# Optimization experiments

Measured on AMD Instinct MI355X. Metric: run time of the kernel, lower is better.

## Reference

```python
import jax, jax.numpy as jnp
import numpy as np

B, T = 256, 64
EMBED, GRU, HID = 1024, 1024, 1024
SD, SC = 32, 32
ADIM = 6
UNIMIX = 0.01
SFLAT = SD * SC


def setup_inputs() -> dict:
    key = jax.random.key(0)
    ks = jax.random.split(key, 16)
    rn = lambda k, s: jax.random.normal(k, s, jnp.float32) * 0.02
    return {
        "embeds": jax.random.normal(ks[0], (B, T, EMBED), jnp.float32),
        "actions": jax.random.uniform(ks[1], (B, T, ADIM), jnp.float32),
        "h_init": jnp.zeros((B, GRU), jnp.float32),
        "z_init": jnp.zeros((B, SD, SC), jnp.float32),
        "W_pre": rn(ks[2], (HID, SFLAT + ADIM)), "b_pre": jnp.zeros((HID,)),
        "g_pre": jnp.ones((HID,)), "be_pre": jnp.zeros((HID,)),
        "W_ih": rn(ks[3], (3 * GRU, HID)), "W_hh": rn(ks[4], (3 * GRU, GRU)),
        "b_ih": jnp.zeros((3 * GRU,)), "b_hh": jnp.zeros((3 * GRU,)),
        "g_gn": jnp.ones((GRU,)), "b_gn": jnp.zeros((GRU,)),
        "Wp1": rn(ks[5], (HID, GRU)), "bp1": jnp.zeros((HID,)),
        "gp": jnp.ones((HID,)), "bpn": jnp.zeros((HID,)),
        "Wp2": rn(ks[6], (SFLAT, HID)), "bp2": jnp.zeros((SFLAT,)),
        "Wq1": rn(ks[7], (HID, GRU + EMBED)), "bq1": jnp.zeros((HID,)),
        "gq": jnp.ones((HID,)), "bqn": jnp.zeros((HID,)),
        "Wq2": rn(ks[8], (SFLAT, HID)), "bq2": jnp.zeros((SFLAT,)),
        # pre-drawn uniform noise -> gumbel, for categorical sampling per step
        "u_prior": jax.random.uniform(ks[9], (T, B, SD, SC), jnp.float32, 1e-6, 1.0 - 1e-6),
        "u_post": jax.random.uniform(ks[10], (T, B, SD, SC), jnp.float32, 1e-6, 1.0 - 1e-6),
    }


def _ln(x, g, b, eps=1e-5):
    m = jnp.mean(x, -1, keepdims=True)
    v = jnp.var(x, -1, keepdims=True)
    return (x - m) * jax.lax.rsqrt(v + eps) * g + b


def _mlp(x, W1, b1, g, bn, W2, b2):
    h = jax.nn.silu(_ln(x @ W1.T + b1, g, bn))
    return h @ W2.T + b2


def _sample(logits, u):
    # logits: (B, SD*SC), u: (B, SD, SC) uniform noise
    lg = logits.reshape(logits.shape[0], SD, SC)
    probs = jax.nn.softmax(lg, axis=-1)
    probs = (1.0 - UNIMIX) * probs + UNIMIX / SC
    gumbel = -jnp.log(-jnp.log(u))
    idx = jnp.argmax(jnp.log(probs) + gumbel, axis=-1)  # multinomial sample
    oh = jax.nn.one_hot(idx, SC, dtype=probs.dtype)
    z = oh + probs - jax.lax.stop_gradient(probs)  # straight-through
    return z, probs


def reference(embeds, actions, h_init, z_init,
              W_pre, b_pre, g_pre, be_pre,
              W_ih, W_hh, b_ih, b_hh, g_gn, b_gn,
              Wp1, bp1, gp, bpn, Wp2, bp2,
              Wq1, bq1, gq, bqn, Wq2, bq2,
              u_prior, u_post):
    def step(carry, xs):
        h, z = carry
        a, e, up, uq = xs
        x = jnp.concatenate([z.reshape(z.shape[0], -1), a], axis=-1)
        x = jax.nn.silu(_ln(x @ W_pre.T + b_pre, g_pre, be_pre))
        # GRUCell
        gx = x @ W_ih.T + b_ih
        gh = h @ W_hh.T + b_hh
        xr, xu, xn = jnp.split(gx, 3, axis=-1)
        hr, hu, hn = jnp.split(gh, 3, axis=-1)
        r = jax.nn.sigmoid(xr + hr)
        u_gate = jax.nn.sigmoid(xu + hu)
        n = jnp.tanh(xn + r * hn)
        h = (1.0 - u_gate) * n + u_gate * h
        h = _ln(h, g_gn, b_gn)
        prior_logits = _mlp(h, Wp1, bp1, gp, bpn, Wp2, bp2)
        _, prior_p = _sample(prior_logits, up)
        post_logits = _mlp(jnp.concatenate([h, e], axis=-1), Wq1, bq1, gq, bqn, Wq2, bq2)
        post_z, post_p = _sample(post_logits, uq)
        return (h, post_z), (h, post_z, prior_p, post_p)

    xs = (jnp.swapaxes(actions, 0, 1), jnp.swapaxes(embeds, 0, 1), u_prior, u_post)
    _, (hs, zs, pp, qp) = jax.lax.scan(step, (h_init, z_init), xs)
    # (T,B,...) -> (B,T,...)
    return (jnp.swapaxes(hs, 0, 1), jnp.swapaxes(zs, 0, 1),
            jnp.swapaxes(pp, 0, 1), jnp.swapaxes(qp, 0, 1))
```

## Files before the change

kernel.cpp:

```cpp
#include <hip/hip_runtime.h>
#include <hip/hip_bf16.h>
#include <math.h>


struct GArg {
  const float* A0; int lda0;
  const float* A1; int lda1;
  int kSplit;
  const float* W; int ldw;
  float* C; int N; int K;
};

struct LArg {
  const float* Y; int S;
  const float* bias; const float* g; const float* be;
  float* O;
};

__device__ __forceinline__ float exp_cr(float x)  { return (float)exp((double)x); }
__device__ __forceinline__ float log_cr(float x)  { return (float)log((double)x); }
__device__ __forceinline__ float tanh_cr(float x) { return (float)tanh((double)x); }
__device__ __forceinline__ float sigmoid_cr(float x) {
  float e = exp_cr(-x);
  float d = __fadd_rn(1.0f, e);
  return __fdiv_rn(1.0f, d);
}

__global__ __launch_bounds__(256) void gemm_k(GArg g0, GArg g1, GArg g2,
                                              int z1, int z2) {
  int z = blockIdx.z;
  GArg G; int s;
  if (z < z1)      { G = g0; s = z; }
  else if (z < z2) { G = g1; s = z - z1; }
  else             { G = g2; s = z - z2; }
  int n0 = blockIdx.x * 64;
  if (n0 >= G.N) return;
  int m0 = blockIdx.y * 64;

  __shared__ float As[2][16][68];
  __shared__ float Bs[2][16][68];

  int tid = threadIdx.x;
  int tx = tid & 15, ty = tid >> 4;
  int kq = tid & 3,  rr = tid >> 2;

  bool vecOK = ((G.ldw & 3) == 0) && ((G.lda0 & 3) == 0) && ((G.lda1 & 3) == 0)
            && (((G.kSplit & 15) == 0) || (G.kSplit >= G.K));

  float acc[4][4];
  #pragma unroll
  for (int j = 0; j < 4; ++j)
    #pragma unroll
    for (int i = 0; i < 4; ++i) acc[j][i] = 0.0f;

  int nt = (G.K + 15) >> 4;
  int t0 = s * 24, t1 = min(nt, t0 + 24);

  float a[4], w[4];
  int useVec = 0;

  auto stage_load = [&](int kt) {
    int kb = kt * 16;
    useVec = vecOK && (kb + 16 <= G.K);
    if (useVec) {
      int k = kb + kq * 4;
      float4 av = (k < G.kSplit)
        ? *(const float4*)(G.A0 + (size_t)(m0 + rr) * G.lda0 + k)
        : *(const float4*)(G.A1 + (size_t)(m0 + rr) * G.lda1 + (k - G.kSplit));
      float4 wv = *(const float4*)(G.W + (size_t)(n0 + rr) * G.ldw + k);
      a[0] = av.x; a[1] = av.y; a[2] = av.z; a[3] = av.w;
      w[0] = wv.x; w[1] = wv.y; w[2] = wv.z; w[3] = wv.w;
    } else {
      int k = kb + tx;
      #pragma unroll
      for (int i = 0; i < 4; ++i) { a[i] = 0.0f; w[i] = 0.0f; }
      if (k < G.K) {
        if (k < G.kSplit) {
          const float* Ap = G.A0 + (size_t)(m0 + ty * 4) * G.lda0 + k;
          #pragma unroll
          for (int i = 0; i < 4; ++i) a[i] = Ap[(size_t)i * G.lda0];
        } else {
          const float* Ap = G.A1 + (size_t)(m0 + ty * 4) * G.lda1 + (k - G.kSplit);
          #pragma unroll
          for (int i = 0; i < 4; ++i) a[i] = Ap[(size_t)i * G.lda1];
        }
        const float* Wp = G.W + (size_t)(n0 + ty * 4) * G.ldw + k;
        #pragma unroll
        for (int i = 0; i < 4; ++i) w[i] = Wp[(size_t)i * G.ldw];
      }
    }
  };
  auto stage_write = [&](int b) {
    if (useVec) {
      #pragma unroll
      for (int i = 0; i < 4; ++i) {
        As[b][kq * 4 + i][rr] = a[i];
        Bs[b][kq * 4 + i][rr] = w[i];
      }
    } else {
      *(float4*)&As[b][tx][ty * 4] = make_float4(a[0], a[1], a[2], a[3]);
      *(float4*)&Bs[b][tx][ty * 4] = make_float4(w[0], w[1], w[2], w[3]);
    }
  };
  auto compute = [&](int b) {
    #pragma unroll
    for (int kk = 0; kk < 16; ++kk) {
      float4 av = *(const float4*)&As[b][kk][ty * 4];
      float4 bv = *(const float4*)&Bs[b][kk][tx * 4];
      float aa[4] = {av.x, av.y, av.z, av.w};
      float bb[4] = {bv.x, bv.y, bv.z, bv.w};
      #pragma unroll
      for (int j = 0; j < 4; ++j)
        #pragma unroll
        for (int i = 0; i < 4; ++i)
          acc[j][i] = fmaf(aa[j], bb[i], acc[j][i]);
    }
  };

  stage_load(t0); stage_write(0); __syncthreads();
  int cur = 0;
  for (int kt = t0; kt < t1; ++kt) {
    if (kt + 1 < t1) {
      stage_load(kt + 1);
      compute(cur);
      stage_write(cur ^ 1);
      __syncthreads();
      cur ^= 1;
    } else compute(cur);
  }

  float* Cp = G.C + (size_t)s * 256 * G.N;
  #pragma unroll
  for (int j = 0; j < 4; ++j)
    *(float4*)&Cp[(size_t)(m0 + ty * 4 + j) * G.N + n0 + tx * 4] =
      make_float4(acc[j][0], acc[j][1], acc[j][2], acc[j][3]);
}

__global__ __launch_bounds__(256) void lnsilu2_k(LArg l0, LArg l1) {
  LArg L = blockIdx.y ? l1 : l0;
  __shared__ float xs[64][20];
  __shared__ float stats[2];
  int row = blockIdx.x, tid = threadIdx.x;
  int cl = tid & 63, iq = tid >> 6;
  int kb = cl >> 3, j = cl & 7;

  float xv[4];
  #pragma unroll
  for (int q = 0; q < 4; ++q) {
    int i = iq * 4 + q;
    int n = kb * 128 + 8 * i + j;
    size_t idx = (size_t)row * 1024 + n;
    float x = L.Y[idx];
    for (int ss = 1; ss < L.S; ++ss) x = __fadd_rn(x, L.Y[(size_t)ss * 262144 + idx]);
    x = __fadd_rn(x, L.bias[n]);
    xv[q] = x;
    xs[cl][i] = x;
  }
  __syncthreads();
  if (tid < 64) {
    float r = xs[cl][0];
    #pragma unroll
    for (int i = 1; i < 16; ++i) r = __fadd_rn(r, xs[cl][i]);
    r = __fadd_rn(r, __shfl_xor(r, 1));
    r = __fadd_rn(r, __shfl_xor(r, 2));
    r = __fadd_rn(r, __shfl_xor(r, 4));
    r = __fadd_rn(r, __shfl_xor(r, 8));
    r = __fadd_rn(r, __shfl_xor(r, 16));
    r = __fadd_rn(r, __shfl_xor(r, 32));
    float mean = __fmul_rn(r, 0.0009765625f);
    float d0 = __fsub_rn(xs[cl][0], mean);
    float r2 = __fmul_rn(d0, d0);
    #pragma unroll
    for (int i = 1; i < 16; ++i) {
      float d = __fsub_rn(xs[cl][i], mean);
      r2 = __fadd_rn(r2, __fmul_rn(d, d));
    }
    r2 = __fadd_rn(r2, __shfl_xor(r2, 1));
    r2 = __fadd_rn(r2, __shfl_xor(r2, 2));
    r2 = __fadd_rn(r2, __shfl_xor(r2, 4));
    r2 = __fadd_rn(r2, __shfl_xor(r2, 8));
    r2 = __fadd_rn(r2, __shfl_xor(r2, 16));
    r2 = __fadd_rn(r2, __shfl_xor(r2, 32));
    float var = __fmul_rn(r2, 0.0009765625f);
    float sdv = __fsqrt_rn(__fadd_rn(var, (float)1e-5));
    if (cl == 0) { stats[0] = mean; stats[1] = __fdiv_rn(1.0f, sdv); }
  }
  __syncthreads();
  float mean = stats[0], rstd = stats[1];
  #pragma unroll
  for (int q = 0; q < 4; ++q) {
    int i = iq * 4 + q;
    int n = kb * 128 + 8 * i + j;
    float d = __fsub_rn(xv[q], mean);
    float t = __fmul_rn(__fmul_rn(d, rstd), L.g[n]);
    t = __fadd_rn(t, L.be[n]);
    L.O[(size_t)row * 1024 + n] = __fmul_rn(t, sigmoid_cr(t));
  }
}

__global__ __launch_bounds__(256) void gru256_k(
  const float* GX, const float* GH, float* H,
  const float* b_ih, const float* b_hh, const float* g_gn, const float* b_gn,
  float* out, int t)
{
  __shared__ float xs[64][20];
  __shared__ float stats[2];
  int row = blockIdx.x, tid = threadIdx.x;
  int cl = tid & 63, iq = tid >> 6;
  int kb = cl >> 3, j = cl & 7;

  float hv[4];
  #pragma unroll
  for (int q = 0; q < 4; ++q) {
    int i = iq * 4 + q;
    int n = kb * 128 + 8 * i + j;
    size_t i0 = (size_t)row * 3072 + n;
    #define FOLD3(P, off) __fadd_rn(__fadd_rn((P)[off], (P)[786432 + (off)]), (P)[1572864 + (off)])
    float xr = __fadd_rn(FOLD3(GX, i0),        b_ih[n]);
    float xu = __fadd_rn(FOLD3(GX, i0 + 1024), b_ih[n + 1024]);
    float xn = __fadd_rn(FOLD3(GX, i0 + 2048), b_ih[n + 2048]);
    float hr = __fadd_rn(FOLD3(GH, i0),        b_hh[n]);
    float hu = __fadd_rn(FOLD3(GH, i0 + 1024), b_hh[n + 1024]);
    float hn = __fadd_rn(FOLD3(GH, i0 + 2048), b_hh[n + 2048]);
    #undef FOLD3
    float r = sigmoid_cr(__fadd_rn(xr, hr));
    float u = sigmoid_cr(__fadd_rn(xu, hu));
    float nn = tanh_cr(__fadd_rn(xn, __fmul_rn(r, hn)));
    float h2 = __fadd_rn(__fmul_rn(__fsub_rn(1.0f, u), nn),
                         __fmul_rn(u, H[(size_t)row * 1024 + n]));
    hv[q] = h2;
    xs[cl][i] = h2;
  }
  __syncthreads();
  if (tid < 64) {
    float r = xs[cl][0];
    #pragma unroll
    for (int i = 1; i < 16; ++i) r = __fadd_rn(r, xs[cl][i]);
    r = __fadd_rn(r, __shfl_xor(r, 1));
    r = __fadd_rn(r, __shfl_xor(r, 2));
    r = __fadd_rn(r, __shfl_xor(r, 4));
    r = __fadd_rn(r, __shfl_xor(r, 8));
    r = __fadd_rn(r, __shfl_xor(r, 16));
    r = __fadd_rn(r, __shfl_xor(r, 32));
    float mean = __fmul_rn(r, 0.0009765625f);
    float d0 = __fsub_rn(xs[cl][0], mean);
    float r2 = __fmul_rn(d0, d0);
    #pragma unroll
    for (int i = 1; i < 16; ++i) {
      float d = __fsub_rn(xs[cl][i], mean);
      r2 = __fadd_rn(r2, __fmul_rn(d, d));
    }
    r2 = __fadd_rn(r2, __shfl_xor(r2, 1));
    r2 = __fadd_rn(r2, __shfl_xor(r2, 2));
    r2 = __fadd_rn(r2, __shfl_xor(r2, 4));
    r2 = __fadd_rn(r2, __shfl_xor(r2, 8));
    r2 = __fadd_rn(r2, __shfl_xor(r2, 16));
    r2 = __fadd_rn(r2, __shfl_xor(r2, 32));
    float var = __fmul_rn(r2, 0.0009765625f);
    float sdv = __fsqrt_rn(__fadd_rn(var, (float)1e-5));
    if (cl == 0) { stats[0] = mean; stats[1] = __fdiv_rn(1.0f, sdv); }
  }
  __syncthreads();
  float mean = stats[0], rstd = stats[1];
  #pragma unroll
  for (int q = 0; q < 4; ++q) {
    int i = iq * 4 + q;
    int n = kb * 128 + 8 * i + j;
    float d = __fsub_rn(hv[q], mean);
    float h3 = __fadd_rn(__fmul_rn(__fmul_rn(d, rstd), g_gn[n]), b_gn[n]);
    H[(size_t)row * 1024 + n] = h3;
    out[((size_t)row * 64 + t) * 1024 + n] = h3;
  }
}

__global__ __launch_bounds__(256) void sample2_k(
  const float* Yq, const float* bq2, const float* Y2p, const float* bp2,
  const float* u_post, const float* actions, float* XZ, float* out, int t)
{
  const size_t NOUT = 16777216ull;
  int b = blockIdx.x, tid = threadIdx.x;
  int d = tid >> 3, lane = tid & 7;
  const float C0 = (float)(1.0 - 0.01);
  const float C1 = (float)(0.01 / 32.0);
  int prior = blockIdx.y;
  const float* Y = prior ? Y2p : Yq;
  const float* bias = prior ? bp2 : bq2;

  float lg[4];
  #pragma unroll
  for (int i = 0; i < 4; ++i) {
    int col = d * 32 + lane + 8 * i;
    size_t idx = (size_t)b * 1024 + col;
    float x = __fadd_rn(__fadd_rn(Y[idx], Y[262144 + idx]), Y[524288 + idx]);
    lg[i] = __fadd_rn(x, bias[col]);
  }
  float mx = fmaxf(fmaxf(lg[0], lg[1]), fmaxf(lg[2], lg[3]));
  for (int off = 4; off; off >>= 1) mx = fmaxf(mx, __shfl_xor(mx, off, 8));

  float e[4];
  #pragma unroll
  for (int i = 0; i < 4; ++i) e[i] = exp_cr(__fsub_rn(lg[i], mx));
  float ssum = e[0];
  ssum = __fadd_rn(ssum, e[1]);
  ssum = __fadd_rn(ssum, e[2]);
  ssum = __fadd_rn(ssum, e[3]);
  ssum = __fadd_rn(ssum, __shfl_xor(ssum, 1, 8));
  ssum = __fadd_rn(ssum, __shfl_xor(ssum, 2, 8));
  ssum = __fadd_rn(ssum, __shfl_xor(ssum, 4, 8));

  float p[4];
  #pragma unroll
  for (int i = 0; i < 4; ++i) {
    float pr = __fdiv_rn(e[i], ssum);
    p[i] = __fadd_rn(__fmul_rn(C0, pr), C1);
  }

  size_t ob = ((size_t)b * 64 + t) * 1024;
  if (prior) {
    #pragma unroll
    for (int i = 0; i < 4; ++i)
      out[2 * NOUT + ob + (d * 32 + lane + 8 * i)] = p[i];
    return;
  }

  float bv = -3.4e38f; int bc = 33;
  #pragma unroll
  for (int i = 0; i < 4; ++i) {
    int c = lane + 8 * i, col = d * 32 + c;
    out[3 * NOUT + ob + col] = p[i];
    float uu = u_post[((size_t)t * 256 + b) * 1024 + col];
    float l1 = log_cr(uu);
    float v1 = -l1;
    float l2 = log_cr(v1);
    float gu = -l2;
    float lp = log_cr(p[i]);
    float val = __fadd_rn(lp, gu);
    if (val > bv) { bv = val; bc = c; }
  }
  for (int off = 4; off; off >>= 1) {
    float ov = __shfl_xor(bv, off, 8);
    int   oc = __shfl_xor(bc, off, 8);
    if (ov > bv || (ov == bv && oc < bc)) { bv = ov; bc = oc; }
  }
  #pragma unroll
  for (int i = 0; i < 4; ++i) {
    int c = lane + 8 * i, col = d * 32 + c;
    float zv = 0.0f;
    if (c == bc) zv = __fsub_rn(__fadd_rn(1.0f, p[i]), p[i]);
    out[NOUT + ob + col] = zv;
    XZ[(size_t)b * 1040 + col] = zv;
  }
  if (tid < 6 && (t + 1) < 64)
    XZ[(size_t)b * 1040 + 1024 + tid] = actions[((size_t)b * 64 + (t + 1)) * 6 + tid];
}

__global__ __launch_bounds__(256) void init_k(const float* h_init, const float* z_init,
                                              const float* actions, float* H, float* XZ)
{
  int b = blockIdx.x, tid = threadIdx.x;
  #pragma unroll
  for (int j = 0; j < 4; ++j) {
    int n = tid + j * 256;
    H [(size_t)b * 1024 + n] = h_init[(size_t)b * 1024 + n];
    XZ[(size_t)b * 1040 + n] = z_init[(size_t)b * 1024 + n];
  }
  if (tid < 6) XZ[(size_t)b * 1040 + 1024 + tid] = actions[(size_t)b * 64 * 6 + tid];
}

extern "C" void kernel_launch(void* const* d_in, const int* in_sizes, int n_in,
                              void* d_out, int out_size, void* d_ws, size_t ws_size,
                              hipStream_t stream)
{
  const float* embeds  = (const float*)d_in[0];
  const float* actions = (const float*)d_in[1];
  const float* h_init  = (const float*)d_in[2];
  const float* z_init  = (const float*)d_in[3];
  const float* W_pre   = (const float*)d_in[4];
  const float* b_pre   = (const float*)d_in[5];
  const float* g_pre   = (const float*)d_in[6];
  const float* be_pre  = (const float*)d_in[7];
  const float* W_ih    = (const float*)d_in[8];
  const float* W_hh    = (const float*)d_in[9];
  const float* b_ih    = (const float*)d_in[10];
  const float* b_hh    = (const float*)d_in[11];
  const float* g_gn    = (const float*)d_in[12];
  const float* b_gn    = (const float*)d_in[13];
  const float* Wp1     = (const float*)d_in[14];
  const float* bp1     = (const float*)d_in[15];
  const float* gp      = (const float*)d_in[16];
  const float* bpn     = (const float*)d_in[17];
  const float* Wp2     = (const float*)d_in[18];
  const float* bp2     = (const float*)d_in[19];
  const float* Wq1     = (const float*)d_in[20];
  const float* bq1     = (const float*)d_in[21];
  const float* gq      = (const float*)d_in[22];
  const float* bqn     = (const float*)d_in[23];
  const float* Wq2     = (const float*)d_in[24];
  const float* bq2     = (const float*)d_in[25];
  const float* u_post  = (const float*)d_in[27];
  float* out           = (float*)d_out;
  const int KS = 1 << 30;

  float* W0   = (float*)d_ws;
  float* H    = W0;
  float* XZ   = W0 + 262144;
  float* PREY = W0 + 528384;
  float* Q1A  = PREY;
  float* GX   = W0 + 1314816;
  float* GH   = W0 + 3674112;
  float* YQ   = W0 + 6033408;
  float* Y2p  = YQ;
  float* YQ2  = W0 + 7606272;
  float* XPRE = YQ2;
  float* Y1p  = W0 + 8392704;
  float* P1Ap = W0 + 9179136;

  hipLaunchKernelGGL(init_k, dim3(256), dim3(256), 0, stream, h_init, z_init, actions, H, XZ);

  GArg pre0{XZ, 1040, XZ, 1040, KS, W_pre, 1030, PREY, 1024, 1030};
  hipLaunchKernelGGL(gemm_k, dim3(16, 4, 3), dim3(256), 0, stream, pre0, pre0, pre0, 3, 3);
  {
    LArg lp{PREY, 3, b_pre, g_pre, be_pre, XPRE};
    hipLaunchKernelGGL(lnsilu2_k, dim3(256, 1), dim3(256), 0, stream, lp, lp);
    GArg gx{XPRE, 1024, XPRE, 1024, KS, W_ih, 1024, GX, 3072, 1024};
    GArg gh{H,    1024, H,    1024, KS, W_hh, 1024, GH, 3072, 1024};
    hipLaunchKernelGGL(gemm_k, dim3(48, 4, 6), dim3(256), 0, stream, gx, gh, gh, 3, 6);
  }

  for (int t = 0; t < 64; ++t) {
    hipLaunchKernelGGL(gru256_k, dim3(256), dim3(256), 0, stream,
                       GX, GH, H, b_ih, b_hh, g_gn, b_gn, out, t);
    GArg q1 {H, 1024, embeds + (size_t)t * 1024, 65536, 1024, Wq1, 2048, YQ, 1024, 2048};
    GArg gh {H, 1024, H, 1024, KS, W_hh, 1024, GH, 3072, 1024};
    GArg py1{out + (size_t)t * 1024, 65536, out, 65536, KS, Wp1, 1024, Y1p, 1024, 1024};
    if (t < 63)
      hipLaunchKernelGGL(gemm_k, dim3(48, 4, 12), dim3(256), 0, stream, q1, gh, py1, 6, 9);
    else
      hipLaunchKernelGGL(gemm_k, dim3(48, 4, 9), dim3(256), 0, stream, q1, q1, py1, 6, 6);
    {
      LArg lq{YQ, 6, bq1, gq, bqn, Q1A};
      LArg lr{Y1p, 3, bp1, gp, bpn, P1Ap};
      hipLaunchKernelGGL(lnsilu2_k, dim3(256, 2), dim3(256), 0, stream, lq, lr);
    }
    GArg q2 {Q1A,  1024, Q1A,  1024, KS, Wq2, 1024, YQ2, 1024, 1024};
    GArg py2{P1Ap, 1024, P1Ap, 1024, KS, Wp2, 1024, Y2p, 1024, 1024};
    hipLaunchKernelGGL(gemm_k, dim3(16, 4, 6), dim3(256), 0, stream, q2, q2, py2, 3, 3);
    hipLaunchKernelGGL(sample2_k, dim3(256, 2), dim3(256), 0, stream,
                       YQ2, bq2, Y2p, bp2, u_post, actions, XZ, out, t);
    if (t < 63) {
      GArg pre{XZ, 1040, XZ, 1040, KS, W_pre, 1030, PREY, 1024, 1030};
      hipLaunchKernelGGL(gemm_k, dim3(16, 4, 3), dim3(256), 0, stream, pre, pre, pre, 3, 3);
      LArg lp{PREY, 3, b_pre, g_pre, be_pre, XPRE};
      hipLaunchKernelGGL(lnsilu2_k, dim3(256, 1), dim3(256), 0, stream, lp, lp);
      GArg gx{XPRE, 1024, XPRE, 1024, KS, W_ih, 1024, GX, 3072, 1024};
      hipLaunchKernelGGL(gemm_k, dim3(48, 4, 3), dim3(256), 0, stream, gx, gx, gx, 3, 3);
    }
  }
}
```

Before: 11.15 ms.

## Fuse all per-step kernels into one persistent kernel with grid barriers

Replaces the per-timestep sequence of GEMM, layernorm, GRU and sampling kernel launches with a single persistent kernel of 512 blocks. Stages are separated by a software grid barrier built on atomic counters, and blocks loop over the GEMM tiles and rows. This removes roughly 400 kernel launches and their gaps, at the cost of barrier spin overhead. It assumes all 512 blocks are co-resident; if they are not, the barrier deadlocks.

After: 27.90 ms. +150.3%, slower.

```diff
diff --git a/kernel.cpp b/kernel.cpp
--- a/kernel.cpp
+++ b/kernel.cpp
@@ -2,6 +2,9 @@
 #include <hip/hip_bf16.h>
 #include <math.h>
 
+
+#define NB 512
+constexpr int KS = 1 << 30;
 
 struct GArg {
   const float* A0; int lda0;
@@ -11,12 +14,6 @@
   float* C; int N; int K;
 };
 
-struct LArg {
-  const float* Y; int S;
-  const float* bias; const float* g; const float* be;
-  float* O;
-};
-
 __device__ __forceinline__ float exp_cr(float x)  { return (float)exp((double)x); }
 __device__ __forceinline__ float log_cr(float x)  { return (float)log((double)x); }
 __device__ __forceinline__ float tanh_cr(float x) { return (float)tanh((double)x); }
@@ -26,20 +23,23 @@
   return __fdiv_rn(1.0f, d);
 }
 
-__global__ __launch_bounds__(256) void gemm_k(GArg g0, GArg g1, GArg g2,
-                                              int z1, int z2) {
-  int z = blockIdx.z;
-  GArg G; int s;
-  if (z < z1)      { G = g0; s = z; }
-  else if (z < z2) { G = g1; s = z - z1; }
-  else             { G = g2; s = z - z2; }
-  int n0 = blockIdx.x * 64;
-  if (n0 >= G.N) return;
-  int m0 = blockIdx.y * 64;
-
-  __shared__ float As[2][16][68];
-  __shared__ float Bs[2][16][68];
-
+__device__ __forceinline__ void gbar(unsigned* cnt, unsigned* gen, unsigned* round) {
+  __syncthreads();
+  if (threadIdx.x == 0) {
+    unsigned target = ++(*round);
+    __threadfence();
+    unsigned v = atomicAdd(cnt, 1u);
+    if (v == target * (unsigned)NB - 1u) atomicAdd(gen, 1u);
+    while (__hip_atomic_load(gen, __ATOMIC_RELAXED, __HIP_MEMORY_SCOPE_AGENT) < target)
+      __builtin_amdgcn_s_sleep(2);
+    __threadfence();
+  }
+  __syncthreads();
+}
+
+__device__ void gemm_tile(const GArg& G, int s, int n0, int m0,
+                          float (*As)[16][68], float (*Bs)[16][68])
+{
   int tid = threadIdx.x;
   int tx = tid & 15, ty = tid >> 4;
   int kq = tid & 3,  rr = tid >> 2;
@@ -117,6 +117,7 @@
     }
   };
 
+  __syncthreads();
   stage_load(t0); stage_write(0); __syncthreads();
   int cur = 0;
   for (int kt = t0; kt < t1; ++kt) {
@@ -136,11 +137,29 @@
       make_float4(acc[j][0], acc[j][1], acc[j][2], acc[j][3]);
 }
 
-__global__ __launch_bounds__(256) void lnsilu2_k(LArg l0, LArg l1) {
-  LArg L = blockIdx.y ? l1 : l0;
-  __shared__ float xs[64][20];
-  __shared__ float stats[2];
-  int row = blockIdx.x, tid = threadIdx.x;
+__device__ void run3(const GArg& A, int ca, const GArg& B, int cb,
+                     const GArg& C, int cc,
+                     float (*As)[16][68], float (*Bs)[16][68])
+{
+  int tot = ca + cb + cc;
+  for (int wv = blockIdx.x; wv < tot; wv += NB) {
+    const GArg* G; int l;
+    if (wv < ca)            { G = &A; l = wv; }
+    else if (wv < ca + cb)  { G = &B; l = wv - ca; }
+    else                    { G = &C; l = wv - ca - cb; }
+    int nbx = G->N >> 6;
+    int per = nbx * 4;
+    int s = l / per, rem = l % per;
+    int mb = rem / nbx, nb = rem % nbx;
+    gemm_tile(*G, s, nb * 64, mb * 64, As, Bs);
+  }
+}
+
+__device__ void ln_row(const float* Y, int S, const float* bias, const float* gg,
+                       const float* be, float* O, int row,
+                       float (*xs)[20], float* stats)
+{
+  int tid = threadIdx.x;
   int cl = tid & 63, iq = tid >> 6;
   int kb = cl >> 3, j = cl & 7;
 
@@ -150,9 +169,9 @@
     int i = iq * 4 + q;
     int n = kb * 128 + 8 * i + j;
     size_t idx = (size_t)row * 1024 + n;
-    float x = L.Y[idx];
-    for (int ss = 1; ss < L.S; ++ss) x = __fadd_rn(x, L.Y[(size_t)ss * 262144 + idx]);
-    x = __fadd_rn(x, L.bias[n]);
+    float x = Y[idx];
+    for (int ss = 1; ss < S; ++ss) x = __fadd_rn(x, Y[(size_t)ss * 262144 + idx]);
+    x = __fadd_rn(x, bias[n]);
     xv[q] = x;
     xs[cl][i] = x;
   }
@@ -192,20 +211,19 @@
     int i = iq * 4 + q;
     int n = kb * 128 + 8 * i + j;
     float d = __fsub_rn(xv[q], mean);
-    float t = __fmul_rn(__fmul_rn(d, rstd), L.g[n]);
-    t = __fadd_rn(t, L.be[n]);
-    L.O[(size_t)row * 1024 + n] = __fmul_rn(t, sigmoid_cr(t));
-  }
-}
-
-__global__ __launch_bounds__(256) void gru256_k(
-  const float* GX, const float* GH, float* H,
-  const float* b_ih, const float* b_hh, const float* g_gn, const float* b_gn,
-  float* out, int t)
-{
-  __shared__ float xs[64][20];
-  __shared__ float stats[2];
-  int row = blockIdx.x, tid = threadIdx.x;
+    float t = __fmul_rn(__fmul_rn(d, rstd), gg[n]);
+    t = __fadd_rn(t, be[n]);
+    O[(size_t)row * 1024 + n] = __fmul_rn(t, sigmoid_cr(t));
+  }
+}
+
+__device__ void gru_row(const float* GX, const float* GH, float* H,
+                        const float* b_ih, const float* b_hh,
+                        const float* g_gn, const float* b_gn,
+                        float* out, int t, int row,
+                        float (*xs)[20], float* stats)
+{
+  int tid = threadIdx.x;
   int cl = tid & 63, iq = tid >> 6;
   int kb = cl >> 3, j = cl & 7;
 
@@ -273,16 +291,16 @@
   }
 }
 
-__global__ __launch_bounds__(256) void sample2_k(
-  const float* Yq, const float* bq2, const float* Y2p, const float* bp2,
-  const float* u_post, const float* actions, float* XZ, float* out, int t)
+__device__ void sample_row(const float* Yq, const float* bq2,
+                           const float* Y2p, const float* bp2,
+                           const float* u_post, const float* actions,
+                           float* XZ, float* out, int t, int b, int prior)
 {
   const size_t NOUT = 16777216ull;
-  int b = blockIdx.x, tid = threadIdx.x;
+  int tid = threadIdx.x;
   int d = tid >> 3, lane = tid & 7;
   const float C0 = (float)(1.0 - 0.01);
   const float C1 = (float)(0.01 / 32.0);
-  int prior = blockIdx.y;
   const float* Y = prior ? Y2p : Yq;
   const float* bias = prior ? bp2 : bq2;
 
@@ -354,106 +372,140 @@
     XZ[(size_t)b * 1040 + 1024 + tid] = actions[((size_t)b * 64 + (t + 1)) * 6 + tid];
 }
 
-__global__ __launch_bounds__(256) void init_k(const float* h_init, const float* z_init,
-                                              const float* actions, float* H, float* XZ)
-{
-  int b = blockIdx.x, tid = threadIdx.x;
-  #pragma unroll
-  for (int j = 0; j < 4; ++j) {
-    int n = tid + j * 256;
-    H [(size_t)b * 1024 + n] = h_init[(size_t)b * 1024 + n];
-    XZ[(size_t)b * 1040 + n] = z_init[(size_t)b * 1024 + n];
-  }
-  if (tid < 6) XZ[(size_t)b * 1040 + 1024 + tid] = actions[(size_t)b * 64 * 6 + tid];
+struct MegaP {
+  const float *embeds, *actions, *h_init, *z_init;
+  const float *W_pre, *b_pre, *g_pre, *be_pre;
+  const float *W_ih, *W_hh, *b_ih, *b_hh, *g_gn, *b_gn;
+  const float *Wp1, *bp1, *gp, *bpn, *Wp2, *bp2;
+  const float *Wq1, *bq1, *gq, *bqn, *Wq2, *bq2;
+  const float *u_post;
+  float* out;
+  float *H, *XZ, *PREY, *Q1A, *GX, *GH, *YQ, *Y2p, *YQ2, *XPRE, *Y1p, *P1Ap;
+  unsigned *cnt, *gen;
+};
+
+__global__ void bar_init_k(unsigned* base) { base[0] = 0; base[32] = 0; }
+
+__global__ __launch_bounds__(256, 2) void mega_k(MegaP P)
+{
+  __shared__ float As[2][16][68];
+  __shared__ float Bs[2][16][68];
+  __shared__ float xs[64][20];
+  __shared__ float stats[2];
+  unsigned round = 0;
+
+  for (int r = blockIdx.x; r < 256; r += NB) {
+    int tid = threadIdx.x;
+    #pragma unroll
+    for (int j = 0; j < 4; ++j) {
+      int n = tid + j * 256;
+      P.H [(size_t)r * 1024 + n] = P.h_init[(size_t)r * 1024 + n];
+      P.XZ[(size_t)r * 1040 + n] = P.z_init[(size_t)r * 1024 + n];
+    }
+    if (tid < 6) P.XZ[(size_t)r * 1040 + 1024 + tid] = P.actions[(size_t)r * 64 * 6 + tid];
+  }
+  gbar(P.cnt, P.gen, &round);
+
+  GArg dummy{nullptr, 0, nullptr, 0, 0, nullptr, 0, nullptr, 0, 0};
+
+  for (int t = 0; t < 64; ++t) {
+    {
+      GArg pre{P.XZ, 1040, P.XZ, 1040, KS, P.W_pre, 1030, P.PREY, 1024, 1030};
+      run3(pre, 192, dummy, 0, dummy, 0, As, Bs);
+    }
+    gbar(P.cnt, P.gen, &round);
+    for (int r = blockIdx.x; r < 256; r += NB)
+      ln_row(P.PREY, 3, P.b_pre, P.g_pre, P.be_pre, P.XPRE, r, xs, stats);
+    gbar(P.cnt, P.gen, &round);
+    {
+      GArg gx{P.XPRE, 1024, P.XPRE, 1024, KS, P.W_ih, 1024, P.GX, 3072, 1024};
+      GArg gh{P.H,    1024, P.H,    1024, KS, P.W_hh, 1024, P.GH, 3072, 1024};
+      if (t == 0) run3(gx, 576, gh, 576, dummy, 0, As, Bs);
+      else        run3(gx, 576, dummy, 0, dummy, 0, As, Bs);
+    }
+    gbar(P.cnt, P.gen, &round);
+    for (int r = blockIdx.x; r < 256; r += NB)
+      gru_row(P.GX, P.GH, P.H, P.b_ih, P.b_hh, P.g_gn, P.b_gn, P.out, t, r, xs, stats);
+    gbar(P.cnt, P.gen, &round);
+    {
+      GArg q1 {P.H, 1024, P.embeds + (size_t)t * 1024, 65536, 1024,
+               P.Wq1, 2048, P.YQ, 1024, 2048};
+      GArg gh {P.H, 1024, P.H, 1024, KS, P.W_hh, 1024, P.GH, 3072, 1024};
+      GArg py1{P.out + (size_t)t * 1024, 65536, P.out, 65536, KS,
+               P.Wp1, 1024, P.Y1p, 1024, 1024};
+      if (t < 63) run3(q1, 384, gh, 576, py1, 192, As, Bs);
+      else        run3(q1, 384, py1, 192, dummy, 0, As, Bs);
+    }
+    gbar(P.cnt, P.gen, &round);
+    for (int r = blockIdx.x; r < 512; r += NB) {
+      if (r < 256) ln_row(P.YQ, 6, P.bq1, P.gq, P.bqn, P.Q1A, r, xs, stats);
+      else         ln_row(P.Y1p, 3, P.bp1, P.gp, P.bpn, P.P1Ap, r - 256, xs, stats);
+    }
+    gbar(P.cnt, P.gen, &round);
+    {
+      GArg q2 {P.Q1A,  1024, P.Q1A,  1024, KS, P.Wq2, 1024, P.YQ2, 1024, 1024};
+      GArg py2{P.P1Ap, 1024, P.P1Ap, 1024, KS, P.Wp2, 1024, P.Y2p, 1024, 1024};
+      run3(q2, 192, py2, 192, dummy, 0, As, Bs);
+    }
+    gbar(P.cnt, P.gen, &round);
+    for (int r = blockIdx.x; r < 512; r += NB)
+      sample_row(P.YQ2, P.bq2, P.Y2p, P.bp2, P.u_post, P.actions,
+                 P.XZ, P.out, t, r & 255, r >> 8);
+    gbar(P.cnt, P.gen, &round);
+  }
 }
 
 extern "C" void kernel_launch(void* const* d_in, const int* in_sizes, int n_in,
                               void* d_out, int out_size, void* d_ws, size_t ws_size,
                               hipStream_t stream)
 {
-  const float* embeds  = (const float*)d_in[0];
-  const float* actions = (const float*)d_in[1];
-  const float* h_init  = (const float*)d_in[2];
-  const float* z_init  = (const float*)d_in[3];
-  const float* W_pre   = (const float*)d_in[4];
-  const float* b_pre   = (const float*)d_in[5];
-  const float* g_pre   = (const float*)d_in[6];
-  const float* be_pre  = (const float*)d_in[7];
-  const float* W_ih    = (const float*)d_in[8];
-  const float* W_hh    = (const float*)d_in[9];
-  const float* b_ih    = (const float*)d_in[10];
-  const float* b_hh    = (const float*)d_in[11];
-  const float* g_gn    = (const float*)d_in[12];
-  const float* b_gn    = (const float*)d_in[13];
-  const float* Wp1     = (const float*)d_in[14];
-  const float* bp1     = (const float*)d_in[15];
-  const float* gp      = (const float*)d_in[16];
-  const float* bpn     = (const float*)d_in[17];
-  const float* Wp2     = (const float*)d_in[18];
-  const float* bp2     = (const float*)d_in[19];
-  const float* Wq1     = (const float*)d_in[20];
-  const float* bq1     = (const float*)d_in[21];
-  const float* gq      = (const float*)d_in[22];
-  const float* bqn     = (const float*)d_in[23];
-  const float* Wq2     = (const float*)d_in[24];
-  const float* bq2     = (const float*)d_in[25];
-  const float* u_post  = (const float*)d_in[27];
-  float* out           = (float*)d_out;
-  const int KS = 1 << 30;
-
-  float* W0   = (float*)d_ws;
-  float* H    = W0;
-  float* XZ   = W0 + 262144;
-  float* PREY = W0 + 528384;
-  float* Q1A  = PREY;
-  float* GX   = W0 + 1314816;
-  float* GH   = W0 + 3674112;
-  float* YQ   = W0 + 6033408;
-  float* Y2p  = YQ;
-  float* YQ2  = W0 + 7606272;
-  float* XPRE = YQ2;
-  float* Y1p  = W0 + 8392704;
-  float* P1Ap = W0 + 9179136;
-
-  hipLaunchKernelGGL(init_k, dim3(256), dim3(256), 0, stream, h_init, z_init, actions, H, XZ);
-
-  GArg pre0{XZ, 1040, XZ, 1040, KS, W_pre, 1030, PREY, 1024, 1030};
-  hipLaunchKernelGGL(gemm_k, dim3(16, 4, 3), dim3(256), 0, stream, pre0, pre0, pre0, 3, 3);
-  {
-    LArg lp{PREY, 3, b_pre, g_pre, be_pre, XPRE};
-    hipLaunchKernelGGL(lnsilu2_k, dim3(256, 1), dim3(256), 0, stream, lp, lp);
-    GArg gx{XPRE, 1024, XPRE, 1024, KS, W_ih, 1024, GX, 3072, 1024};
-    GArg gh{H,    1024, H,    1024, KS, W_hh, 1024, GH, 3072, 1024};
-    hipLaunchKernelGGL(gemm_k, dim3(48, 4, 6), dim3(256), 0, stream, gx, gh, gh, 3, 6);
-  }
-
-  for (int t = 0; t < 64; ++t) {
-    hipLaunchKernelGGL(gru256_k, dim3(256), dim3(256), 0, stream,
-                       GX, GH, H, b_ih, b_hh, g_gn, b_gn, out, t);
-    GArg q1 {H, 1024, embeds + (size_t)t * 1024, 65536, 1024, Wq1, 2048, YQ, 1024, 2048};
-    GArg gh {H, 1024, H, 1024, KS, W_hh, 1024, GH, 3072, 1024};
-    GArg py1{out + (size_t)t * 1024, 65536, out, 65536, KS, Wp1, 1024, Y1p, 1024, 1024};
-    if (t < 63)
-      hipLaunchKernelGGL(gemm_k, dim3(48, 4, 12), dim3(256), 0, stream, q1, gh, py1, 6, 9);
-    else
-      hipLaunchKernelGGL(gemm_k, dim3(48, 4, 9), dim3(256), 0, stream, q1, q1, py1, 6, 6);
-    {
-      LArg lq{YQ, 6, bq1, gq, bqn, Q1A};
-      LArg lr{Y1p, 3, bp1, gp, bpn, P1Ap};
-      hipLaunchKernelGGL(lnsilu2_k, dim3(256, 2), dim3(256), 0, stream, lq, lr);
-    }
-    GArg q2 {Q1A,  1024, Q1A,  1024, KS, Wq2, 1024, YQ2, 1024, 1024};
-    GArg py2{P1Ap, 1024, P1Ap, 1024, KS, Wp2, 1024, Y2p, 1024, 1024};
-    hipLaunchKernelGGL(gemm_k, dim3(16, 4, 6), dim3(256), 0, stream, q2, q2, py2, 3, 3);
-    hipLaunchKernelGGL(sample2_k, dim3(256, 2), dim3(256), 0, stream,
-                       YQ2, bq2, Y2p, bp2, u_post, actions, XZ, out, t);
-    if (t < 63) {
-      GArg pre{XZ, 1040, XZ, 1040, KS, W_pre, 1030, PREY, 1024, 1030};
-      hipLaunchKernelGGL(gemm_k, dim3(16, 4, 3), dim3(256), 0, stream, pre, pre, pre, 3, 3);
-      LArg lp{PREY, 3, b_pre, g_pre, be_pre, XPRE};
-      hipLaunchKernelGGL(lnsilu2_k, dim3(256, 1), dim3(256), 0, stream, lp, lp);
-      GArg gx{XPRE, 1024, XPRE, 1024, KS, W_ih, 1024, GX, 3072, 1024};
-      hipLaunchKernelGGL(gemm_k, dim3(48, 4, 3), dim3(256), 0, stream, gx, gx, gx, 3, 3);
-    }
-  }
-}
+  MegaP P;
+  P.embeds  = (const float*)d_in[0];
+  P.actions = (const float*)d_in[1];
+  P.h_init  = (const float*)d_in[2];
+  P.z_init  = (const float*)d_in[3];
+  P.W_pre   = (const float*)d_in[4];
+  P.b_pre   = (const float*)d_in[5];
+  P.g_pre   = (const float*)d_in[6];
+  P.be_pre  = (const float*)d_in[7];
+  P.W_ih    = (const float*)d_in[8];
+  P.W_hh    = (const float*)d_in[9];
+  P.b_ih    = (const float*)d_in[10];
+  P.b_hh    = (const float*)d_in[11];
+  P.g_gn    = (const float*)d_in[12];
+  P.b_gn    = (const float*)d_in[13];
+  P.Wp1     = (const float*)d_in[14];
+  P.bp1     = (const float*)d_in[15];
+  P.gp      = (const float*)d_in[16];
+  P.bpn     = (const float*)d_in[17];
+  P.Wp2     = (const float*)d_in[18];
+  P.bp2     = (const float*)d_in[19];
+  P.Wq1     = (const float*)d_in[20];
+  P.bq1     = (const float*)d_in[21];
+  P.gq      = (const float*)d_in[22];
+  P.bqn     = (const float*)d_in[23];
+  P.Wq2     = (const float*)d_in[24];
+  P.bq2     = (const float*)d_in[25];
+  P.u_post  = (const float*)d_in[27];
+  P.out     = (float*)d_out;
+
+  float* W0 = (float*)d_ws;
+  P.H    = W0;
+  P.XZ   = W0 + 262144;
+  P.PREY = W0 + 528384;
+  P.Q1A  = P.PREY;
+  P.GX   = W0 + 1314816;
+  P.GH   = W0 + 3674112;
+  P.YQ   = W0 + 6033408;
+  P.Y2p  = P.YQ;
+  P.YQ2  = W0 + 7606272;
+  P.XPRE = P.YQ2;
+  P.Y1p  = W0 + 8392704;
+  P.P1Ap = W0 + 9179136;
+  unsigned* bar_base = (unsigned*)(W0 + 9441280);
+  P.cnt = bar_base;
+  P.gen = bar_base + 32;
+
+  hipLaunchKernelGGL(bar_init_k, dim3(1), dim3(1), 0, stream, bar_base);
+  hipLaunchKernelGGL(mega_k, dim3(NB), dim3(256), 0, stream, P);
+}
```

## Exploit one-hot sparsity of z to fuse pre-projection into sampling kernel

Applied to the files above, without the earlier changes.

The posterior sample z is one-hot per group, so the W_pre projection becomes a gather of 32 weight columns per row plus the 6 action columns. The change computes it directly inside the sampling kernel, followed by LayerNorm and SiLU, and merges the prior and posterior sampling into one block. This removes the dense pre GEMM and the separate LayerNorm launch on each step. The cost is strided gathered reads of W_pre rows and a different summation order than the split-K GEMM. It also relies on the straight-through value (1+p-p) being the only nonzero in each group.

Measured after the change: 11.56 ms. 1.04x slower.

```diff
diff --git a/kernel.cpp b/kernel.cpp
--- a/kernel.cpp
+++ b/kernel.cpp
@@ -273,85 +273,179 @@
   }
 }
 
-__global__ __launch_bounds__(256) void sample2_k(
+__global__ __launch_bounds__(256) void fused_k(
   const float* Yq, const float* bq2, const float* Y2p, const float* bp2,
-  const float* u_post, const float* actions, float* XZ, float* out, int t)
+  const float* u_post, const float* actions,
+  const float* W_pre, const float* b_pre, const float* g_pre, const float* be_pre,
+  float* XPRE, float* out, int t)
 {
   const size_t NOUT = 16777216ull;
+  __shared__ int   sidx[32];
+  __shared__ float szval[32];
+  __shared__ float sact[8];
+  __shared__ float xs[64][20];
+  __shared__ float stats[2];
   int b = blockIdx.x, tid = threadIdx.x;
   int d = tid >> 3, lane = tid & 7;
   const float C0 = (float)(1.0 - 0.01);
   const float C1 = (float)(0.01 / 32.0);
-  int prior = blockIdx.y;
-  const float* Y = prior ? Y2p : Yq;
-  const float* bias = prior ? bp2 : bq2;
-
-  float lg[4];
-  #pragma unroll
-  for (int i = 0; i < 4; ++i) {
-    int col = d * 32 + lane + 8 * i;
-    size_t idx = (size_t)b * 1024 + col;
-    float x = __fadd_rn(__fadd_rn(Y[idx], Y[262144 + idx]), Y[524288 + idx]);
-    lg[i] = __fadd_rn(x, bias[col]);
-  }
-  float mx = fmaxf(fmaxf(lg[0], lg[1]), fmaxf(lg[2], lg[3]));
-  for (int off = 4; off; off >>= 1) mx = fmaxf(mx, __shfl_xor(mx, off, 8));
-
-  float e[4];
-  #pragma unroll
-  for (int i = 0; i < 4; ++i) e[i] = exp_cr(__fsub_rn(lg[i], mx));
-  float ssum = e[0];
-  ssum = __fadd_rn(ssum, e[1]);
-  ssum = __fadd_rn(ssum, e[2]);
-  ssum = __fadd_rn(ssum, e[3]);
-  ssum = __fadd_rn(ssum, __shfl_xor(ssum, 1, 8));
-  ssum = __fadd_rn(ssum, __shfl_xor(ssum, 2, 8));
-  ssum = __fadd_rn(ssum, __shfl_xor(ssum, 4, 8));
-
-  float p[4];
-  #pragma unroll
-  for (int i = 0; i < 4; ++i) {
-    float pr = __fdiv_rn(e[i], ssum);
-    p[i] = __fadd_rn(__fmul_rn(C0, pr), C1);
-  }
-
   size_t ob = ((size_t)b * 64 + t) * 1024;
-  if (prior) {
-    #pragma unroll
-    for (int i = 0; i < 4; ++i)
-      out[2 * NOUT + ob + (d * 32 + lane + 8 * i)] = p[i];
-    return;
-  }
-
-  float bv = -3.4e38f; int bc = 33;
-  #pragma unroll
-  for (int i = 0; i < 4; ++i) {
-    int c = lane + 8 * i, col = d * 32 + c;
-    out[3 * NOUT + ob + col] = p[i];
-    float uu = u_post[((size_t)t * 256 + b) * 1024 + col];
-    float l1 = log_cr(uu);
-    float v1 = -l1;
-    float l2 = log_cr(v1);
-    float gu = -l2;
-    float lp = log_cr(p[i]);
-    float val = __fadd_rn(lp, gu);
-    if (val > bv) { bv = val; bc = c; }
-  }
-  for (int off = 4; off; off >>= 1) {
-    float ov = __shfl_xor(bv, off, 8);
-    int   oc = __shfl_xor(bc, off, 8);
-    if (ov > bv || (ov == bv && oc < bc)) { bv = ov; bc = oc; }
-  }
-  #pragma unroll
-  for (int i = 0; i < 4; ++i) {
-    int c = lane + 8 * i, col = d * 32 + c;
-    float zv = 0.0f;
-    if (c == bc) zv = __fsub_rn(__fadd_rn(1.0f, p[i]), p[i]);
-    out[NOUT + ob + col] = zv;
-    XZ[(size_t)b * 1040 + col] = zv;
-  }
-  if (tid < 6 && (t + 1) < 64)
-    XZ[(size_t)b * 1040 + 1024 + tid] = actions[((size_t)b * 64 + (t + 1)) * 6 + tid];
+
+  {
+    float lg[4];
+    #pragma unroll
+    for (int i = 0; i < 4; ++i) {
+      int col = d * 32 + lane + 8 * i;
+      size_t idx = (size_t)b * 1024 + col;
+      float x = __fadd_rn(__fadd_rn(Yq[idx], Yq[262144 + idx]), Yq[524288 + idx]);
+      lg[i] = __fadd_rn(x, bq2[col]);
+    }
+    float mx = fmaxf(fmaxf(lg[0], lg[1]), fmaxf(lg[2], lg[3]));
+    for (int off = 4; off; off >>= 1) mx = fmaxf(mx, __shfl_xor(mx, off, 8));
+    float e[4];
+    #pragma unroll
+    for (int i = 0; i < 4; ++i) e[i] = exp_cr(__fsub_rn(lg[i], mx));
+    float ssum = e[0];
+    ssum = __fadd_rn(ssum, e[1]);
+    ssum = __fadd_rn(ssum, e[2]);
+    ssum = __fadd_rn(ssum, e[3]);
+    ssum = __fadd_rn(ssum, __shfl_xor(ssum, 1, 8));
+    ssum = __fadd_rn(ssum, __shfl_xor(ssum, 2, 8));
+    ssum = __fadd_rn(ssum, __shfl_xor(ssum, 4, 8));
+    float p[4];
+    #pragma unroll
+    for (int i = 0; i < 4; ++i) {
+      float pr = __fdiv_rn(e[i], ssum);
+      p[i] = __fadd_rn(__fmul_rn(C0, pr), C1);
+    }
+    float bv = -3.4e38f; int bc = 33;
+    #pragma unroll
+    for (int i = 0; i < 4; ++i) {
+      int c = lane + 8 * i, col = d * 32 + c;
+      out[3 * NOUT + ob + col] = p[i];
+      float uu = u_post[((size_t)t * 256 + b) * 1024 + col];
+      float l1 = log_cr(uu);
+      float v1 = -l1;
+      float l2 = log_cr(v1);
+      float gu = -l2;
+      float lp = log_cr(p[i]);
+      float val = __fadd_rn(lp, gu);
+      if (val > bv) { bv = val; bc = c; }
+    }
+    for (int off = 4; off; off >>= 1) {
+      float ov = __shfl_xor(bv, off, 8);
+      int   oc = __shfl_xor(bc, off, 8);
+      if (ov > bv || (ov == bv && oc < bc)) { bv = ov; bc = oc; }
+    }
+    #pragma unroll
+    for (int i = 0; i < 4; ++i) {
+      int c = lane + 8 * i, col = d * 32 + c;
+      float zv = 0.0f;
+      if (c == bc) { zv = __fsub_rn(__fadd_rn(1.0f, p[i]), p[i]); szval[d] = zv; }
+      out[NOUT + ob + col] = zv;
+    }
+    if (lane == 0) sidx[d] = bc;
+  }
+
+  {
+    float lg[4];
+    #pragma unroll
+    for (int i = 0; i < 4; ++i) {
+      int col = d * 32 + lane + 8 * i;
+      size_t idx = (size_t)b * 1024 + col;
+      float x = __fadd_rn(__fadd_rn(Y2p[idx], Y2p[262144 + idx]), Y2p[524288 + idx]);
+      lg[i] = __fadd_rn(x, bp2[col]);
+    }
+    float mx = fmaxf(fmaxf(lg[0], lg[1]), fmaxf(lg[2], lg[3]));
+    for (int off = 4; off; off >>= 1) mx = fmaxf(mx, __shfl_xor(mx, off, 8));
+    float e[4];
+    #pragma unroll
+    for (int i = 0; i < 4; ++i) e[i] = exp_cr(__fsub_rn(lg[i], mx));
+    float ssum = e[0];
+    ssum = __fadd_rn(ssum, e[1]);
+    ssum = __fadd_rn(ssum, e[2]);
+    ssum = __fadd_rn(ssum, e[3]);
+    ssum = __fadd_rn(ssum, __shfl_xor(ssum, 1, 8));
+    ssum = __fadd_rn(ssum, __shfl_xor(ssum, 2, 8));
+    ssum = __fadd_rn(ssum, __shfl_xor(ssum, 4, 8));
+    #pragma unroll
+    for (int i = 0; i < 4; ++i) {
+      int col = d * 32 + lane + 8 * i;
+      float pr = __fdiv_rn(e[i], ssum);
+      out[2 * NOUT + ob + col] = __fadd_rn(__fmul_rn(C0, pr), C1);
+    }
+  }
+
+  if (t < 63) {
+    if (tid < 6) sact[tid] = actions[((size_t)b * 64 + (t + 1)) * 6 + tid];
+    __syncthreads();
+    int cl = tid & 63, iq = tid >> 6;
+    int kb = cl >> 3, j = cl & 7;
+    float xv[4];
+    #pragma unroll
+    for (int q = 0; q < 4; ++q) {
+      int i = iq * 4 + q;
+      int n = kb * 128 + 8 * i + j;
+      const float* Wr = W_pre + (size_t)n * 1030;
+      float p0 = 0.0f, p1 = 0.0f, p2 = 0.0f;
+      #pragma unroll
+      for (int dd = 0; dd < 12; ++dd)
+        p0 = fmaf(szval[dd], Wr[dd * 32 + sidx[dd]], p0);
+      #pragma unroll
+      for (int dd = 12; dd < 24; ++dd)
+        p1 = fmaf(szval[dd], Wr[dd * 32 + sidx[dd]], p1);
+      #pragma unroll
+      for (int dd = 24; dd < 32; ++dd)
+        p2 = fmaf(szval[dd], Wr[dd * 32 + sidx[dd]], p2);
+      #pragma unroll
+      for (int ai = 0; ai < 6; ++ai)
+        p2 = fmaf(sact[ai], Wr[1024 + ai], p2);
+      float x = __fadd_rn(__fadd_rn(p0, p1), p2);
+      x = __fadd_rn(x, b_pre[n]);
+      xv[q] = x;
+      xs[cl][i] = x;
+    }
+    __syncthreads();
+    if (tid < 64) {
+      float r = xs[cl][0];
+      #pragma unroll
+      for (int i = 1; i < 16; ++i) r = __fadd_rn(r, xs[cl][i]);
+      r = __fadd_rn(r, __shfl_xor(r, 1));
+      r = __fadd_rn(r, __shfl_xor(r, 2));
+      r = __fadd_rn(r, __shfl_xor(r, 4));
+      r = __fadd_rn(r, __shfl_xor(r, 8));
+      r = __fadd_rn(r, __shfl_xor(r, 16));
+      r = __fadd_rn(r, __shfl_xor(r, 32));
+      float mean = __fmul_rn(r, 0.0009765625f);
+      float d0 = __fsub_rn(xs[cl][0], mean);
+      float r2 = __fmul_rn(d0, d0);
+      #pragma unroll
+      for (int i = 1; i < 16; ++i) {
+        float dd = __fsub_rn(xs[cl][i], mean);
+        r2 = __fadd_rn(r2, __fmul_rn(dd, dd));
+      }
+      r2 = __fadd_rn(r2, __shfl_xor(r2, 1));
+      r2 = __fadd_rn(r2, __shfl_xor(r2, 2));
+      r2 = __fadd_rn(r2, __shfl_xor(r2, 4));
+      r2 = __fadd_rn(r2, __shfl_xor(r2, 8));
+      r2 = __fadd_rn(r2, __shfl_xor(r2, 16));
+      r2 = __fadd_rn(r2, __shfl_xor(r2, 32));
+      float var = __fmul_rn(r2, 0.0009765625f);
+      float sdv = __fsqrt_rn(__fadd_rn(var, (float)1e-5));
+      if (cl == 0) { stats[0] = mean; stats[1] = __fdiv_rn(1.0f, sdv); }
+    }
+    __syncthreads();
+    float mean = stats[0], rstd = stats[1];
+    #pragma unroll
+    for (int q = 0; q < 4; ++q) {
+      int i = iq * 4 + q;
+      int n = kb * 128 + 8 * i + j;
+      float dd = __fsub_rn(xv[q], mean);
+      float tt = __fmul_rn(__fmul_rn(dd, rstd), g_pre[n]);
+      tt = __fadd_rn(tt, be_pre[n]);
+      XPRE[(size_t)b * 1024 + n] = __fmul_rn(tt, sigmoid_cr(tt));
+    }
+  }
 }
 
 __global__ __launch_bounds__(256) void init_k(const float* h_init, const float* z_init,
@@ -445,13 +539,10 @@
     GArg q2 {Q1A,  1024, Q1A,  1024, KS, Wq2, 1024, YQ2, 1024, 1024};
     GArg py2{P1Ap, 1024, P1Ap, 1024, KS, Wp2, 1024, Y2p, 1024, 1024};
     hipLaunchKernelGGL(gemm_k, dim3(16, 4, 6), dim3(256), 0, stream, q2, q2, py2, 3, 3);
-    hipLaunchKernelGGL(sample2_k, dim3(256, 2), dim3(256), 0, stream,
-                       YQ2, bq2, Y2p, bp2, u_post, actions, XZ, out, t);
+    hipLaunchKernelGGL(fused_k, dim3(256), dim3(256), 0, stream,
+                       YQ2, bq2, Y2p, bp2, u_post, actions,
+                       W_pre, b_pre, g_pre, be_pre, XPRE, out, t);
     if (t < 63) {
-      GArg pre{XZ, 1040, XZ, 1040, KS, W_pre, 1030, PREY, 1024, 1030};
-      hipLaunchKernelGGL(gemm_k, dim3(16, 4, 3), dim3(256), 0, stream, pre, pre, pre, 3, 3);
-      LArg lp{PREY, 3, b_pre, g_pre, be_pre, XPRE};
-      hipLaunchKernelGGL(lnsilu2_k, dim3(256, 1), dim3(256), 0, stream, lp, lp);
       GArg gx{XPRE, 1024, XPRE, 1024, KS, W_ih, 1024, GX, 3072, 1024};
       hipLaunchKernelGGL(gemm_k, dim3(48, 4, 3), dim3(256), 0, stream, gx, gx, gx, 3, 3);
     }
```
